# Performance work log

Measured on AMD Instinct MI355X. Metric: run time of the kernel, lower is better.

Reference implementation:

```python
import jax, jax.numpy as jnp
import numpy as np

N = 50000   # nodes
E = 800000  # edges
IN, H, OUT = 64, 512, 128


def _lin_init(key, out_dim, in_dim):
    kw, kb = jax.random.split(key)
    bound = 1.0 / np.sqrt(in_dim)
    W = jax.random.uniform(kw, (out_dim, in_dim), jnp.float32, -bound, bound)
    b = jax.random.uniform(kb, (out_dim,), jnp.float32, -bound, bound)
    return W, b


def setup_inputs() -> dict:
    key = jax.random.key(0)
    ks = jax.random.split(key, 10)
    x = jax.random.normal(ks[0], (N, IN), jnp.float32)
    edge_index = jax.random.randint(ks[1], (2, E), 0, N, jnp.int64)
    W_s1, b_s1 = _lin_init(ks[2], H, IN)
    W_s2, b_s2 = _lin_init(ks[3], H, H)
    W_s3, b_s3 = _lin_init(ks[4], H, H)
    W_s4, b_s4 = _lin_init(ks[5], H, H)
    W_m1, b_m1 = _lin_init(ks[6], OUT, H)
    W_m2, b_m2 = _lin_init(ks[7], OUT, OUT)
    W_l1, b_l1 = _lin_init(ks[8], OUT, H)
    W_l2, b_l2 = _lin_init(ks[9], OUT, OUT)
    return {"x": x, "edge_index": edge_index,
            "W_s1": W_s1, "b_s1": b_s1, "W_s2": W_s2, "b_s2": b_s2,
            "W_s3": W_s3, "b_s3": b_s3, "W_s4": W_s4, "b_s4": b_s4,
            "W_m1": W_m1, "b_m1": b_m1, "W_m2": W_m2, "b_m2": b_m2,
            "W_l1": W_l1, "b_l1": b_l1, "W_l2": W_l2, "b_l2": b_l2}


def _aggregate(h, src, dst):
    # GINConv with default eps=0: (1+eps)*x + sum_{j in N(i)} x_j
    return h + jax.ops.segment_sum(h[src], dst, num_segments=N)


def reference(x, edge_index,
              W_s1, b_s1, W_s2, b_s2, W_s3, b_s3, W_s4, b_s4,
              W_m1, b_m1, W_m2, b_m2, W_l1, b_l1, W_l2, b_l2):
    src, dst = edge_index[0], edge_index[1]
    lrelu = lambda v: jax.nn.leaky_relu(v, 0.1)

    def mlp_shared(h):
        h = lrelu(h @ W_s1.T + b_s1)
        h = lrelu(h @ W_s2.T + b_s2)
        h = lrelu(h @ W_s3.T + b_s3)
        return h @ W_s4.T + b_s4

    def mlp_mu(h):
        return jax.nn.relu(h @ W_m1.T + b_m1) @ W_m2.T + b_m2

    def mlp_logvar(h):
        return jax.nn.relu(h @ W_l1.T + b_l1) @ W_l2.T + b_l2

    h = jax.nn.relu(mlp_shared(_aggregate(x, src, dst)))
    mu = mlp_mu(_aggregate(h, src, dst))
    logvar = mlp_logvar(_aggregate(h, src, dst))
    return (mu, logvar)
```

## Files before the change

### kernel.cpp

```cpp
#include <hip/hip_runtime.h>
#include <hip/hip_bf16.h>
#include <stdint.h>

#define N_NODES 50000
#define N_PAD   50048
#define E_EDGES 800000
#define MT      391

typedef __bf16 bf16x8 __attribute__((ext_vector_type(8)));
typedef __bf16 bf16x4 __attribute__((ext_vector_type(4)));
typedef float  f32x4  __attribute__((ext_vector_type(4)));

__global__ void count_deg(const int* __restrict__ ei, int* __restrict__ cnt) {
    int e = blockIdx.x * blockDim.x + threadIdx.x;
    if (e < E_EDGES) atomicAdd(&cnt[ei[E_EDGES + e]], 1);
}

#define SCAN_B 1024
__global__ void scan_block(const int* __restrict__ cnt, int* __restrict__ ptr,
                           int* __restrict__ bsum, int n) {
    __shared__ int buf[SCAN_B];
    int i = blockIdx.x * SCAN_B + threadIdx.x;
    int v = (i < n) ? cnt[i] : 0;
    buf[threadIdx.x] = v;
    __syncthreads();
    #pragma unroll
    for (int off = 1; off < SCAN_B; off <<= 1) {
        int t = (threadIdx.x >= (unsigned)off) ? buf[threadIdx.x - off] : 0;
        __syncthreads();
        buf[threadIdx.x] += t;
        __syncthreads();
    }
    if (i < n) ptr[i] = buf[threadIdx.x] - v;
    if (threadIdx.x == SCAN_B - 1) bsum[blockIdx.x] = buf[SCAN_B - 1];
}

__global__ void scan_bsums(int* __restrict__ bsum, int* __restrict__ boff, int nb,
                           int* __restrict__ total_out) {
    __shared__ int buf[64];
    int v = ((int)threadIdx.x < nb) ? bsum[threadIdx.x] : 0;
    buf[threadIdx.x] = v;
    __syncthreads();
    #pragma unroll
    for (int off = 1; off < 64; off <<= 1) {
        int t = (threadIdx.x >= (unsigned)off) ? buf[threadIdx.x - off] : 0;
        __syncthreads();
        buf[threadIdx.x] += t;
        __syncthreads();
    }
    if ((int)threadIdx.x < nb) boff[threadIdx.x] = buf[threadIdx.x] - v;
    if (threadIdx.x == 63) *total_out = buf[63];
}

__global__ void scan_add(int* __restrict__ ptr, const int* __restrict__ boff, int n) {
    int i = blockIdx.x * SCAN_B + threadIdx.x;
    if (i < n) ptr[i] += boff[blockIdx.x];
}

__global__ void fill_csr(const int* __restrict__ ei, const int* __restrict__ ptr,
                         int* __restrict__ cursor, int* __restrict__ col) {
    int e = blockIdx.x * blockDim.x + threadIdx.x;
    if (e < E_EDGES) {
        int dst = ei[E_EDGES + e];
        int pos = ptr[dst] + atomicAdd(&cursor[dst], 1);
        col[pos] = ei[e];
    }
}

#define XN      3200000
#define WTOT    983040
__global__ void cvt_all(const float* __restrict__ x,
                        const float* __restrict__ Ws1, const float* __restrict__ Ws2,
                        const float* __restrict__ Ws3, const float* __restrict__ Ws4,
                        const float* __restrict__ Wm1, const float* __restrict__ Wl1,
                        const float* __restrict__ Wm2, const float* __restrict__ Wl2,
                        __bf16* __restrict__ xb, __bf16* __restrict__ wbuf) {
    int i = blockIdx.x * blockDim.x + threadIdx.x;
    if (i < XN) { xb[i] = (__bf16)x[i]; return; }
    int j = i - XN;
    if (j >= WTOT) return;
    const float* s; int o;
    if      (j <  32768) { s = Ws1; o = j; }
    else if (j < 294912) { s = Ws2; o = j -  32768; }
    else if (j < 557056) { s = Ws3; o = j - 294912; }
    else if (j < 819200) { s = Ws4; o = j - 557056; }
    else if (j < 884736) { s = Wm1; o = j - 819200; }
    else if (j < 950272) { s = Wl1; o = j - 884736; }
    else if (j < 966656) { s = Wm2; o = j - 950272; }
    else                 { s = Wl2; o = j - 966656; }
    wbuf[j] = (__bf16)s[o];
}

__global__ void agg0_gather(const __bf16* __restrict__ xb, const int* __restrict__ ptr,
                            const int* __restrict__ col, __bf16* __restrict__ out) {
    int node = blockIdx.x * 4 + (threadIdx.x >> 6);
    int lane = threadIdx.x & 63;
    if (node >= N_PAD) return;
    long o = (long)node * 64 + lane;
    if (node >= N_NODES) { out[o] = (__bf16)0.0f; return; }
    float acc = (float)xb[o];
    int e0 = ptr[node], e1 = ptr[node + 1];
    int e = e0;
    for (; e + 8 <= e1; e += 8) {
        int c[8];
        #pragma unroll
        for (int u = 0; u < 8; ++u) c[u] = col[e + u];
        float v[8];
        #pragma unroll
        for (int u = 0; u < 8; ++u) v[u] = (float)xb[(long)c[u] * 64 + lane];
        #pragma unroll
        for (int u = 0; u < 8; ++u) acc += v[u];
    }
    for (; e < e1; ++e) acc += (float)xb[(long)col[e] * 64 + lane];
    out[o] = (__bf16)acc;
}

__global__ void aggt_gather(const __bf16* __restrict__ t, const int* __restrict__ ptr,
                            const int* __restrict__ col, const float* __restrict__ b_m1,
                            const float* __restrict__ b_l1, __bf16* __restrict__ p) {
    int node = blockIdx.x * 4 + (threadIdx.x >> 6);
    int lane = threadIdx.x & 63;
    if (node >= N_NODES) return;
    const int f0 = lane * 4;
    bf16x4 s = *(const bf16x4*)&t[(long)node * 256 + f0];
    float a0 = (float)s[0], a1 = (float)s[1], a2 = (float)s[2], a3 = (float)s[3];
    int e0 = ptr[node], e1 = ptr[node + 1];
    int e = e0;
    for (; e + 8 <= e1; e += 8) {
        int c[8];
        #pragma unroll
        for (int u = 0; u < 8; ++u) c[u] = col[e + u];
        bf16x4 v[8];
        #pragma unroll
        for (int u = 0; u < 8; ++u) v[u] = *(const bf16x4*)&t[(long)c[u] * 256 + f0];
        #pragma unroll
        for (int u = 0; u < 8; ++u) {
            a0 += (float)v[u][0]; a1 += (float)v[u][1];
            a2 += (float)v[u][2]; a3 += (float)v[u][3];
        }
    }
    for (; e < e1; ++e) {
        bf16x4 v = *(const bf16x4*)&t[(long)col[e] * 256 + f0];
        a0 += (float)v[0]; a1 += (float)v[1]; a2 += (float)v[2]; a3 += (float)v[3];
    }
    float b0, b1, b2, b3;
    if (f0 < 128) { b0 = b_m1[f0]; b1 = b_m1[f0+1]; b2 = b_m1[f0+2]; b3 = b_m1[f0+3]; }
    else          { b0 = b_l1[f0-128]; b1 = b_l1[f0-127]; b2 = b_l1[f0-126]; b3 = b_l1[f0-125]; }
    bf16x4 r;
    r[0] = (__bf16)fmaxf(a0 + b0, 0.0f);
    r[1] = (__bf16)fmaxf(a1 + b1, 0.0f);
    r[2] = (__bf16)fmaxf(a2 + b2, 0.0f);
    r[3] = (__bf16)fmaxf(a3 + b3, 0.0f);
    *(bf16x4*)&p[(long)node * 256 + f0] = r;
}

__device__ __forceinline__ void gl_lds16(const __bf16* g, __bf16* l) {
    __builtin_amdgcn_global_load_lds(
        (const __attribute__((address_space(1))) uint32_t*)g,
        (__attribute__((address_space(3))) uint32_t*)l, 16, 0, 0);
}

template <int NCOL>
__device__ __forceinline__ void swizzle_xy(int bid, int& x, int& y) {
    int grp  = bid / (8 * NCOL);
    int rem  = bid - grp * (8 * NCOL);
    int base = grp * 8;
    int width = MT - base; if (width > 8) width = 8;
    x = base + rem % width;
    y = rem / width;
}

template <int ACT, bool BIAS, bool OUT_BF16, bool MCHK>
__device__ __forceinline__ void gemm_core(
    const __bf16* __restrict__ A, int lda, const __bf16* __restrict__ W,
    const float* __restrict__ bias, void* __restrict__ Cout, int ldc,
    int K, long Mstore, long blockRow, int blockCol,
    __bf16* __restrict__ smem) {
    __bf16* As = smem;
    __bf16* Ws = smem + 8192;
    const int tid  = threadIdx.x;
    const int wid  = tid >> 6;
    const int lane = tid & 63;
    const int wm = (wid >> 1) << 6;
    const int wn = (wid & 1) << 6;

    f32x4 acc[4][4];
    #pragma unroll
    for (int i = 0; i < 4; ++i)
        #pragma unroll
        for (int j = 0; j < 4; ++j) acc[i][j] = (f32x4)0.0f;

    const int srow = lane >> 3;
    const int skg  = (lane & 7) ^ srow;
    const __bf16* gA[4]; const __bf16* gW[4];
    __bf16 *lA[4], *lW[4];
    #pragma unroll
    for (int i = 0; i < 4; ++i) {
        int c = wid * 4 + i;
        gA[i] = A + (blockRow + c * 8 + srow) * (long)lda + skg * 8;
        gW[i] = W + ((long)blockCol + c * 8 + srow) * (long)K + skg * 8;
        lA[i] = As + c * 512;
        lW[i] = Ws + c * 512;
    }

    const int rA = lane & 15;
    const int q  = lane >> 4;
    const int r7 = rA & 7;

    for (int k0 = 0; k0 < K; k0 += 64) {
        #pragma unroll
        for (int i = 0; i < 4; ++i) gl_lds16(gA[i] + k0, lA[i]);
        #pragma unroll
        for (int i = 0; i < 4; ++i) gl_lds16(gW[i] + k0, lW[i]);
        __syncthreads();

        #pragma unroll
        for (int s = 0; s < 2; ++s) {
            const int slot = ((s * 4 + q) ^ r7) * 8;
            bf16x8 af[4], bf[4];
            #pragma unroll
            for (int mi = 0; mi < 4; ++mi)
                af[mi] = *(const bf16x8*)&As[(wm + mi * 16 + rA) * 64 + slot];
            #pragma unroll
            for (int ni = 0; ni < 4; ++ni)
                bf[ni] = *(const bf16x8*)&Ws[(wn + ni * 16 + rA) * 64 + slot];
            #pragma unroll
            for (int mi = 0; mi < 4; ++mi)
                #pragma unroll
                for (int ni = 0; ni < 4; ++ni)
                    acc[mi][ni] = __builtin_amdgcn_mfma_f32_16x16x32_bf16(
                        af[mi], bf[ni], acc[mi][ni], 0, 0, 0);
        }
        __syncthreads();
    }

    const int ccol = lane & 15;
    const int crow = (lane >> 4) << 2;
    if (OUT_BF16 && !MCHK) {
        #pragma unroll
        for (int mi = 0; mi < 4; ++mi) {
            #pragma unroll
            for (int ni = 0; ni < 4; ++ni) {
                int gc = wn + ni * 16 + ccol;
                float bv = BIAS ? bias[blockCol + gc] : 0.0f;
                #pragma unroll
                for (int r = 0; r < 4; ++r) {
                    float v = acc[mi][ni][r] + bv;
                    if (ACT == 1) v = (v > 0.0f) ? v : 0.1f * v;
                    else if (ACT == 2) v = fmaxf(v, 0.0f);
                    smem[(wm + mi * 16 + crow + r) * 128 + gc] = (__bf16)v;
                }
            }
        }
        __syncthreads();
        #pragma unroll
        for (int i = 0; i < 8; ++i) {
            int o   = (i * 256 + tid) * 8;
            int row = o >> 7;
            int co  = o & 127;
            *(bf16x8*)((__bf16*)Cout + (blockRow + row) * (long)ldc + blockCol + co) =
                *(const bf16x8*)&smem[o];
        }
    } else {
        #pragma unroll
        for (int mi = 0; mi < 4; ++mi) {
            #pragma unroll
            for (int ni = 0; ni < 4; ++ni) {
                long gr0 = blockRow + wm + mi * 16 + crow;
                int  gc  = blockCol + wn + ni * 16 + ccol;
                float bv = BIAS ? bias[gc] : 0.0f;
                #pragma unroll
                for (int r = 0; r < 4; ++r) {
                    long gr = gr0 + r;
                    if (!MCHK || gr < Mstore) {
                        float v = acc[mi][ni][r] + bv;
                        if (ACT == 1) v = (v > 0.0f) ? v : 0.1f * v;
                        else if (ACT == 2) v = fmaxf(v, 0.0f);
                        if (OUT_BF16) ((__bf16*)Cout)[gr * ldc + gc] = (__bf16)v;
                        else          ((float*)Cout)[gr * ldc + gc] = v;
                    }
                }
            }
        }
    }
}

template <int NCOL, int ACT, bool BIAS, bool OUT_BF16, bool MCHK>
__global__ __launch_bounds__(256) void gemm_bt(
    const __bf16* __restrict__ A, int lda, const __bf16* __restrict__ W,
    const float* __restrict__ bias, void* __restrict__ Cout, int ldc,
    int K, long Mstore) {
    __shared__ __bf16 smem[128 * 128];
    int x, y;
    swizzle_xy<NCOL>(blockIdx.x, x, y);
    gemm_core<ACT, BIAS, OUT_BF16, MCHK>(A, lda, W, bias, Cout, ldc, K, Mstore,
                                         (long)x * 128, y * 128, smem);
}

__global__ __launch_bounds__(256) void gemm_heads(
    const __bf16* __restrict__ p, const __bf16* __restrict__ wm2,
    const float* __restrict__ b_m2, float* __restrict__ mu,
    const __bf16* __restrict__ wl2, const float* __restrict__ b_l2,
    float* __restrict__ lv) {
    __shared__ __bf16 smem[128 * 128];
    int x, hd;
    swizzle_xy<2>(blockIdx.x, x, hd);
    if (hd == 0)
        gemm_core<0, true, false, true>(p, 256, wm2, b_m2, mu, 128, 128, N_NODES,
                                        (long)x * 128, 0, smem);
    else
        gemm_core<0, true, false, true>(p + 128, 256, wl2, b_l2, lv, 128, 128, N_NODES,
                                        (long)x * 128, 0, smem);
}

extern "C" void kernel_launch(void* const* d_in, const int* in_sizes, int n_in,
                              void* d_out, int out_size, void* d_ws, size_t ws_size,
                              hipStream_t stream) {
    const float* x    = (const float*)d_in[0];
    const int*   ei   = (const int*)d_in[1];
    const float* W_s1 = (const float*)d_in[2];
    const float* b_s1 = (const float*)d_in[3];
    const float* W_s2 = (const float*)d_in[4];
    const float* b_s2 = (const float*)d_in[5];
    const float* W_s3 = (const float*)d_in[6];
    const float* b_s3 = (const float*)d_in[7];
    const float* W_s4 = (const float*)d_in[8];
    const float* b_s4 = (const float*)d_in[9];
    const float* W_m1 = (const float*)d_in[10];
    const float* b_m1 = (const float*)d_in[11];
    const float* W_m2 = (const float*)d_in[12];
    const float* b_m2 = (const float*)d_in[13];
    const float* W_l1 = (const float*)d_in[14];
    const float* b_l1 = (const float*)d_in[15];
    const float* W_l2 = (const float*)d_in[16];
    const float* b_l2 = (const float*)d_in[17];

    char* ws = (char*)d_ws;
    size_t off = 0;
    auto carve = [&](size_t bytes) -> void* {
        void* p = ws + off;
        off = (off + bytes + 255) & ~(size_t)255;
        return p;
    };
    int* cnt  = (int*)carve((size_t)N_NODES * 4);
    int* cur  = (int*)carve((size_t)N_NODES * 4);
    int* ptr  = (int*)carve((size_t)(N_NODES + 1) * 4);
    int* col  = (int*)carve((size_t)E_EDGES * 4);
    int* bsum = (int*)carve(64 * 4);
    int* boff = (int*)carve(64 * 4);
    __bf16* wbuf = (__bf16*)carve((size_t)WTOT * 2);
    __bf16* w1  = wbuf;
    __bf16* w2  = wbuf +  32768;
    __bf16* w3  = wbuf + 294912;
    __bf16* w4  = wbuf + 557056;
    __bf16* wml = wbuf + 819200;
    __bf16* wm2 = wbuf + 950272;
    __bf16* wl2 = wbuf + 966656;
    __bf16* xb    = (__bf16*)carve((size_t)XN * 2);
    __bf16* agg0b = (__bf16*)carve((size_t)N_PAD * 64 * 2);
    __bf16* B1    = (__bf16*)carve((size_t)N_PAD * 512 * 2);
    __bf16* B2    = (__bf16*)carve((size_t)N_PAD * 512 * 2);

    (void)hipMemsetAsync(cnt, 0, (size_t)N_NODES * 4, stream);
    (void)hipMemsetAsync(cur, 0, (size_t)N_NODES * 4, stream);

    const int NB = (N_NODES + SCAN_B - 1) / SCAN_B;
    count_deg<<<E_EDGES / 256, 256, 0, stream>>>(ei, cnt);
    scan_block<<<NB, SCAN_B, 0, stream>>>(cnt, ptr, bsum, N_NODES);
    scan_bsums<<<1, 64, 0, stream>>>(bsum, boff, NB, &ptr[N_NODES]);
    scan_add<<<NB, SCAN_B, 0, stream>>>(ptr, boff, N_NODES);
    fill_csr<<<E_EDGES / 256, 256, 0, stream>>>(ei, ptr, cur, col);

    cvt_all<<<(XN + WTOT + 255) / 256, 256, 0, stream>>>(
        x, W_s1, W_s2, W_s3, W_s4, W_m1, W_l1, W_m2, W_l2, xb, wbuf);

    agg0_gather<<<N_PAD / 4, 256, 0, stream>>>(xb, ptr, col, agg0b);

    gemm_bt<4, 1, true, true, false><<<MT * 4, 256, 0, stream>>>(agg0b, 64, w1, b_s1, B1, 512, 64, N_PAD);
    gemm_bt<4, 1, true, true, false><<<MT * 4, 256, 0, stream>>>(B1, 512, w2, b_s2, B2, 512, 512, N_PAD);
    gemm_bt<4, 1, true, true, false><<<MT * 4, 256, 0, stream>>>(B2, 512, w3, b_s3, B1, 512, 512, N_PAD);
    gemm_bt<4, 2, true, true, false><<<MT * 4, 256, 0, stream>>>(B1, 512, w4, b_s4, B2, 512, 512, N_PAD);

    __bf16* t = B1;
    gemm_bt<2, 0, false, true, false><<<MT * 2, 256, 0, stream>>>(B2, 512, wml, nullptr, t, 256, 512, N_PAD);

    __bf16* p = B2;
    aggt_gather<<<(N_NODES + 3) / 4, 256, 0, stream>>>(t, ptr, col, b_m1, b_l1, p);

    float* mu = (float*)d_out;
    float* lv = mu + (size_t)N_NODES * 128;
    gemm_heads<<<MT * 2, 256, 0, stream>>>(p, wm2, b_m2, mu, wl2, b_l2, lv);
}
```

Before: 497.8 us.

## Bucket CSR edges by source range and vectorize neighbor gathers

Builds the CSR with a composite key (dst, src>>12), so each node's neighbor list is grouped into 16 source-index buckets. The intent is that concurrent gathers hit nearby rows and get better cache locality. Both aggregation kernels are rewritten to use 16-byte bf16x8 loads. agg0 spreads 8 edges across lane groups and combines them with shuffle reductions, and aggt uses 32 lanes per node with masked tail handling. In exchange, the counting and scan now cover 800k keys instead of 50k, and the count/cursor scratch reuses the B1/B2 buffers.

```diff
diff --git a/kernel.cpp b/kernel.cpp
--- a/kernel.cpp
+++ b/kernel.cpp
@@ -7,13 +7,21 @@
 #define E_EDGES 800000
 #define MT      391
 
+#define NBK       16
+#define SRC_SHIFT 12
+#define NKEY      (N_NODES * NBK)
+
 typedef __bf16 bf16x8 __attribute__((ext_vector_type(8)));
 typedef __bf16 bf16x4 __attribute__((ext_vector_type(4)));
 typedef float  f32x4  __attribute__((ext_vector_type(4)));
 
 __global__ void count_deg(const int* __restrict__ ei, int* __restrict__ cnt) {
     int e = blockIdx.x * blockDim.x + threadIdx.x;
-    if (e < E_EDGES) atomicAdd(&cnt[ei[E_EDGES + e]], 1);
+    if (e < E_EDGES) {
+        int src = ei[e];
+        int dst = ei[E_EDGES + e];
+        atomicAdd(&cnt[dst * NBK + (src >> SRC_SHIFT)], 1);
+    }
 }
 
 #define SCAN_B 1024
@@ -35,21 +43,21 @@
     if (threadIdx.x == SCAN_B - 1) bsum[blockIdx.x] = buf[SCAN_B - 1];
 }
 
-__global__ void scan_bsums(int* __restrict__ bsum, int* __restrict__ boff, int nb,
-                           int* __restrict__ total_out) {
-    __shared__ int buf[64];
+__global__ void scan_bsums(const int* __restrict__ bsum, int* __restrict__ boff,
+                           int nb, int* __restrict__ total_out) {
+    __shared__ int buf[SCAN_B];
     int v = ((int)threadIdx.x < nb) ? bsum[threadIdx.x] : 0;
     buf[threadIdx.x] = v;
     __syncthreads();
     #pragma unroll
-    for (int off = 1; off < 64; off <<= 1) {
+    for (int off = 1; off < SCAN_B; off <<= 1) {
         int t = (threadIdx.x >= (unsigned)off) ? buf[threadIdx.x - off] : 0;
         __syncthreads();
         buf[threadIdx.x] += t;
         __syncthreads();
     }
     if ((int)threadIdx.x < nb) boff[threadIdx.x] = buf[threadIdx.x] - v;
-    if (threadIdx.x == 63) *total_out = buf[63];
+    if (threadIdx.x == SCAN_B - 1) *total_out = buf[SCAN_B - 1];
 }
 
 __global__ void scan_add(int* __restrict__ ptr, const int* __restrict__ boff, int n) {
@@ -57,13 +65,15 @@
     if (i < n) ptr[i] += boff[blockIdx.x];
 }
 
-__global__ void fill_csr(const int* __restrict__ ei, const int* __restrict__ ptr,
+__global__ void fill_csr(const int* __restrict__ ei, const int* __restrict__ ptr2,
                          int* __restrict__ cursor, int* __restrict__ col) {
     int e = blockIdx.x * blockDim.x + threadIdx.x;
     if (e < E_EDGES) {
+        int src = ei[e];
         int dst = ei[E_EDGES + e];
-        int pos = ptr[dst] + atomicAdd(&cursor[dst], 1);
-        col[pos] = ei[e];
+        int key = dst * NBK + (src >> SRC_SHIFT);
+        int pos = ptr2[key] + atomicAdd(&cursor[key], 1);
+        col[pos] = src;
     }
 }
 
@@ -91,67 +101,117 @@
     wbuf[j] = (__bf16)s[o];
 }
 
-__global__ void agg0_gather(const __bf16* __restrict__ xb, const int* __restrict__ ptr,
-                            const int* __restrict__ col, __bf16* __restrict__ out) {
+__global__ __launch_bounds__(256) void agg0_gather(
+    const __bf16* __restrict__ xb, const int* __restrict__ ptr2,
+    const int* __restrict__ col, __bf16* __restrict__ out) {
     int node = blockIdx.x * 4 + (threadIdx.x >> 6);
     int lane = threadIdx.x & 63;
+    int g    = lane >> 3;
+    int f0   = (lane & 7) << 3;
     if (node >= N_PAD) return;
-    long o = (long)node * 64 + lane;
-    if (node >= N_NODES) { out[o] = (__bf16)0.0f; return; }
-    float acc = (float)xb[o];
-    int e0 = ptr[node], e1 = ptr[node + 1];
+    long o = (long)node * 64 + f0;
+    if (node >= N_NODES) {
+        if (g == 0) {
+            bf16x8 z;
+            #pragma unroll
+            for (int i = 0; i < 8; ++i) z[i] = (__bf16)0.0f;
+            *(bf16x8*)&out[o] = z;
+        }
+        return;
+    }
+    float a[8];
+    #pragma unroll
+    for (int i = 0; i < 8; ++i) a[i] = 0.0f;
+    if (g == 0) {
+        bf16x8 s = *(const bf16x8*)&xb[o];
+        #pragma unroll
+        for (int i = 0; i < 8; ++i) a[i] = (float)s[i];
+    }
+    int e0 = ptr2[node * NBK], e1 = ptr2[node * NBK + NBK];
+    int e = e0;
+    for (; e + 16 <= e1; e += 16) {
+        int c0 = col[e + g];
+        int c1 = col[e + 8 + g];
+        bf16x8 v0 = *(const bf16x8*)&xb[(c0 << 6) + f0];
+        bf16x8 v1 = *(const bf16x8*)&xb[(c1 << 6) + f0];
+        #pragma unroll
+        for (int i = 0; i < 8; ++i) a[i] += (float)v0[i] + (float)v1[i];
+    }
+    int rem = e1 - e;
+    if (rem > 0) {
+        int u0 = (g < rem) ? g : 0;        float m0 = (g < rem) ? 1.0f : 0.0f;
+        int i1 = g + 8;
+        int u1 = (i1 < rem) ? i1 : 0;      float m1 = (i1 < rem) ? 1.0f : 0.0f;
+        int c0 = col[e + u0];
+        int c1 = col[e + u1];
+        bf16x8 v0 = *(const bf16x8*)&xb[(c0 << 6) + f0];
+        bf16x8 v1 = *(const bf16x8*)&xb[(c1 << 6) + f0];
+        #pragma unroll
+        for (int i = 0; i < 8; ++i) a[i] += m0 * (float)v0[i] + m1 * (float)v1[i];
+    }
+    #pragma unroll
+    for (int i = 0; i < 8; ++i) {
+        a[i] += __shfl_xor(a[i], 8, 64);
+        a[i] += __shfl_xor(a[i], 16, 64);
+        a[i] += __shfl_xor(a[i], 32, 64);
+    }
+    if (g == 0) {
+        bf16x8 r;
+        #pragma unroll
+        for (int i = 0; i < 8; ++i) r[i] = (__bf16)a[i];
+        *(bf16x8*)&out[o] = r;
+    }
+}
+
+__global__ __launch_bounds__(256) void aggt_gather(
+    const __bf16* __restrict__ t, const int* __restrict__ ptr2,
+    const int* __restrict__ col, const float* __restrict__ b_m1,
+    const float* __restrict__ b_l1, __bf16* __restrict__ p) {
+    int node = blockIdx.x * 8 + (threadIdx.x >> 5);
+    if (node >= N_NODES) return;
+    int hl = threadIdx.x & 31;
+    int f0 = hl << 3;
+    float a[8];
+    {
+        bf16x8 s = *(const bf16x8*)&t[(node << 8) + f0];
+        #pragma unroll
+        for (int i = 0; i < 8; ++i) a[i] = (float)s[i];
+    }
+    int e0 = ptr2[node * NBK], e1 = ptr2[node * NBK + NBK];
     int e = e0;
     for (; e + 8 <= e1; e += 8) {
         int c[8];
         #pragma unroll
         for (int u = 0; u < 8; ++u) c[u] = col[e + u];
-        float v[8];
-        #pragma unroll
-        for (int u = 0; u < 8; ++u) v[u] = (float)xb[(long)c[u] * 64 + lane];
-        #pragma unroll
-        for (int u = 0; u < 8; ++u) acc += v[u];
-    }
-    for (; e < e1; ++e) acc += (float)xb[(long)col[e] * 64 + lane];
-    out[o] = (__bf16)acc;
-}
-
-__global__ void aggt_gather(const __bf16* __restrict__ t, const int* __restrict__ ptr,
-                            const int* __restrict__ col, const float* __restrict__ b_m1,
-                            const float* __restrict__ b_l1, __bf16* __restrict__ p) {
-    int node = blockIdx.x * 4 + (threadIdx.x >> 6);
-    int lane = threadIdx.x & 63;
-    if (node >= N_NODES) return;
-    const int f0 = lane * 4;
-    bf16x4 s = *(const bf16x4*)&t[(long)node * 256 + f0];
-    float a0 = (float)s[0], a1 = (float)s[1], a2 = (float)s[2], a3 = (float)s[3];
-    int e0 = ptr[node], e1 = ptr[node + 1];
-    int e = e0;
-    for (; e + 8 <= e1; e += 8) {
-        int c[8];
-        #pragma unroll
-        for (int u = 0; u < 8; ++u) c[u] = col[e + u];
-        bf16x4 v[8];
-        #pragma unroll
-        for (int u = 0; u < 8; ++u) v[u] = *(const bf16x4*)&t[(long)c[u] * 256 + f0];
-        #pragma unroll
-        for (int u = 0; u < 8; ++u) {
-            a0 += (float)v[u][0]; a1 += (float)v[u][1];
-            a2 += (float)v[u][2]; a3 += (float)v[u][3];
-        }
-    }
-    for (; e < e1; ++e) {
-        bf16x4 v = *(const bf16x4*)&t[(long)col[e] * 256 + f0];
-        a0 += (float)v[0]; a1 += (float)v[1]; a2 += (float)v[2]; a3 += (float)v[3];
-    }
-    float b0, b1, b2, b3;
-    if (f0 < 128) { b0 = b_m1[f0]; b1 = b_m1[f0+1]; b2 = b_m1[f0+2]; b3 = b_m1[f0+3]; }
-    else          { b0 = b_l1[f0-128]; b1 = b_l1[f0-127]; b2 = b_l1[f0-126]; b3 = b_l1[f0-125]; }
-    bf16x4 r;
-    r[0] = (__bf16)fmaxf(a0 + b0, 0.0f);
-    r[1] = (__bf16)fmaxf(a1 + b1, 0.0f);
-    r[2] = (__bf16)fmaxf(a2 + b2, 0.0f);
-    r[3] = (__bf16)fmaxf(a3 + b3, 0.0f);
-    *(bf16x4*)&p[(long)node * 256 + f0] = r;
+        bf16x8 v[8];
+        #pragma unroll
+        for (int u = 0; u < 8; ++u) v[u] = *(const bf16x8*)&t[(c[u] << 8) + f0];
+        #pragma unroll
+        for (int u = 0; u < 8; ++u)
+            #pragma unroll
+            for (int i = 0; i < 8; ++i) a[i] += (float)v[u][i];
+    }
+    int rem = e1 - e;
+    if (rem > 0) {
+        #pragma unroll
+        for (int u = 0; u < 7; ++u) {
+            int   uu = (u < rem) ? u : 0;
+            float m  = (u < rem) ? 1.0f : 0.0f;
+            int   cc = col[e + uu];
+            bf16x8 v = *(const bf16x8*)&t[(cc << 8) + f0];
+            #pragma unroll
+            for (int i = 0; i < 8; ++i) a[i] += m * (float)v[i];
+        }
+    }
+    const float* bp = (f0 < 128) ? (b_m1 + f0) : (b_l1 + (f0 - 128));
+    f32x4 b0 = *(const f32x4*)bp;
+    f32x4 b1 = *(const f32x4*)(bp + 4);
+    bf16x8 r;
+    #pragma unroll
+    for (int i = 0; i < 4; ++i) r[i]     = (__bf16)fmaxf(a[i]     + b0[i], 0.0f);
+    #pragma unroll
+    for (int i = 0; i < 4; ++i) r[4 + i] = (__bf16)fmaxf(a[4 + i] + b1[i], 0.0f);
+    *(bf16x8*)&p[(node << 8) + f0] = r;
 }
 
 __device__ __forceinline__ void gl_lds16(const __bf16* g, __bf16* l) {
@@ -342,12 +402,10 @@
         off = (off + bytes + 255) & ~(size_t)255;
         return p;
     };
-    int* cnt  = (int*)carve((size_t)N_NODES * 4);
-    int* cur  = (int*)carve((size_t)N_NODES * 4);
-    int* ptr  = (int*)carve((size_t)(N_NODES + 1) * 4);
+    int* ptr2 = (int*)carve((size_t)(NKEY + 1) * 4);
     int* col  = (int*)carve((size_t)E_EDGES * 4);
-    int* bsum = (int*)carve(64 * 4);
-    int* boff = (int*)carve(64 * 4);
+    int* bsum = (int*)carve(SCAN_B * 4);
+    int* boff = (int*)carve(SCAN_B * 4);
     __bf16* wbuf = (__bf16*)carve((size_t)WTOT * 2);
     __bf16* w1  = wbuf;
     __bf16* w2  = wbuf +  32768;
@@ -361,20 +419,23 @@
     __bf16* B1    = (__bf16*)carve((size_t)N_PAD * 512 * 2);
     __bf16* B2    = (__bf16*)carve((size_t)N_PAD * 512 * 2);
 
-    (void)hipMemsetAsync(cnt, 0, (size_t)N_NODES * 4, stream);
-    (void)hipMemsetAsync(cur, 0, (size_t)N_NODES * 4, stream);
-
-    const int NB = (N_NODES + SCAN_B - 1) / SCAN_B;
-    count_deg<<<E_EDGES / 256, 256, 0, stream>>>(ei, cnt);
-    scan_block<<<NB, SCAN_B, 0, stream>>>(cnt, ptr, bsum, N_NODES);
-    scan_bsums<<<1, 64, 0, stream>>>(bsum, boff, NB, &ptr[N_NODES]);
-    scan_add<<<NB, SCAN_B, 0, stream>>>(ptr, boff, N_NODES);
-    fill_csr<<<E_EDGES / 256, 256, 0, stream>>>(ei, ptr, cur, col);
+    int* cnt2 = (int*)B1;
+    int* cur2 = (int*)B2;
+
+    (void)hipMemsetAsync(cnt2, 0, (size_t)NKEY * 4, stream);
+    (void)hipMemsetAsync(cur2, 0, (size_t)NKEY * 4, stream);
+
+    const int NB2 = (NKEY + SCAN_B - 1) / SCAN_B;
+    count_deg<<<E_EDGES / 256, 256, 0, stream>>>(ei, cnt2);
+    scan_block<<<NB2, SCAN_B, 0, stream>>>(cnt2, ptr2, bsum, NKEY);
+    scan_bsums<<<1, SCAN_B, 0, stream>>>(bsum, boff, NB2, &ptr2[NKEY]);
+    scan_add<<<NB2, SCAN_B, 0, stream>>>(ptr2, boff, NKEY);
+    fill_csr<<<E_EDGES / 256, 256, 0, stream>>>(ei, ptr2, cur2, col);
 
     cvt_all<<<(XN + WTOT + 255) / 256, 256, 0, stream>>>(
         x, W_s1, W_s2, W_s3, W_s4, W_m1, W_l1, W_m2, W_l2, xb, wbuf);
 
-    agg0_gather<<<N_PAD / 4, 256, 0, stream>>>(xb, ptr, col, agg0b);
+    agg0_gather<<<N_PAD / 4, 256, 0, stream>>>(xb, ptr2, col, agg0b);
 
     gemm_bt<4, 1, true, true, false><<<MT * 4, 256, 0, stream>>>(agg0b, 64, w1, b_s1, B1, 512, 64, N_PAD);
     gemm_bt<4, 1, true, true, false><<<MT * 4, 256, 0, stream>>>(B1, 512, w2, b_s2, B2, 512, 512, N_PAD);
@@ -385,7 +446,7 @@
     gemm_bt<2, 0, false, true, false><<<MT * 2, 256, 0, stream>>>(B2, 512, wml, nullptr, t, 256, 512, N_PAD);
 
     __bf16* p = B2;
-    aggt_gather<<<(N_NODES + 3) / 4, 256, 0, stream>>>(t, ptr, col, b_m1, b_l1, p);
+    aggt_gather<<<(N_NODES + 7) / 8, 256, 0, stream>>>(t, ptr2, col, b_m1, b_l1, p);
 
     float* mu = (float*)d_out;
     float* lv = mu + (size_t)N_NODES * 128;
```

Result: faster. 485.1 us (-2.6%).
